# Optimization experiments

Measured on AMD Instinct MI355X. Metric: run time of the kernel, lower is better.

## Reference

```python
import jax, jax.numpy as jnp
import numpy as np

H = 128
B, N, K = 2, 16384, 16


def _gather_neighbors(a, idx):
    # a: (B,N,D), idx: (B,N,K) -> (B,N,K,D), per-batch gather along N
    return jax.vmap(lambda ab, ib: ab[ib])(a, idx)


def setup_inputs() -> dict:
    key = jax.random.key(0)
    ks = jax.random.split(key, 16)
    def lin(k, fan_in, shape):
        lim = 1.0 / np.sqrt(fan_in)
        return jax.random.uniform(k, shape, jnp.float32, -lim, lim)
    inp = {
        'h': jax.random.normal(ks[0], (B, N, H), jnp.float32),
        'x': jax.random.normal(ks[1], (B, N, 3), jnp.float32),
        'edge_idx': jax.random.randint(ks[2], (B, N, K), 0, N),
        # edge_mlp: Linear(2H+1->H), SiLU, Linear(H->H), SiLU
        'We1': lin(ks[3], 2 * H + 1, (2 * H + 1, H)), 'be1': lin(ks[4], 2 * H + 1, (H,)),
        'We2': lin(ks[5], H, (H, H)), 'be2': lin(ks[6], H, (H,)),
        # coord_mlp: Linear(H->H), SiLU, Linear(H->1, no bias)
        'Wc1': lin(ks[7], H, (H, H)), 'bc1': lin(ks[8], H, (H,)),
        'Wc2': lin(ks[9], H, (H, 1)),
        # node_mlp: Linear(2H->H), SiLU, Linear(H->H)
        'Wn1': lin(ks[10], 2 * H, (2 * H, H)), 'bn1': lin(ks[11], 2 * H, (H,)),
        'Wn2': lin(ks[12], H, (H, H)), 'bn2': lin(ks[13], H, (H,)),
    }
    return inp


def reference(h, x, edge_idx, We1, be1, We2, be2, Wc1, bc1, Wc2, Wn1, bn1, Wn2, bn2):
    k = edge_idx.shape[2]
    h_neigh = _gather_neighbors(h, edge_idx)          # (B,N,K,H)
    x_neigh = _gather_neighbors(x, edge_idx)          # (B,N,K,3)
    x_diff = x[:, :, None, :] - x_neigh               # (B,N,K,3)
    sq_dist = jnp.sum(x_diff * x_diff, axis=-1, keepdims=True)  # (B,N,K,1)
    h_i = jnp.broadcast_to(h[:, :, None, :], h_neigh.shape)
    edge_feat = jnp.concatenate([h_i, h_neigh, sq_dist], axis=-1)  # (B,N,K,2H+1)
    m_ij = jax.nn.silu(jax.nn.silu(edge_feat @ We1 + be1) @ We2 + be2)  # (B,N,K,H)
    coord_w = jax.nn.silu(m_ij @ Wc1 + bc1) @ Wc2     # (B,N,K,1)
    x_new = x + jnp.mean(x_diff * coord_w, axis=2)    # (B,N,3)
    m_i = jnp.sum(m_ij, axis=2)                       # (B,N,H)
    node_in = jnp.concatenate([h, m_i], axis=-1)      # (B,N,2H)
    h_new = jax.nn.silu(node_in @ Wn1 + bn1) @ Wn2 + bn2 + h
    return (h_new, x_new)
```

## Files before the change

### kernel.cpp

```cpp
#include <hip/hip_runtime.h>
#include <hip/hip_bf16.h>
#include <math.h>

#define H 128
#define KN 16
#define NN 16384
#define NB 8
#define EB 128
#define HS 136

typedef short s16x8 __attribute__((ext_vector_type(8)));
typedef float f32x4 __attribute__((ext_vector_type(4)));

__device__ __forceinline__ float u2f_lo(uint u){
    union { uint i; float f; } v; v.i = u << 16; return v.f;
}
__device__ __forceinline__ float u2f_hi(uint u){
    union { uint i; float f; } v; v.i = u & 0xffff0000u; return v.f;
}
__device__ __forceinline__ float b2f(ushort u){
    union { uint i; float f; } v; v.i = ((uint)u) << 16; return v.f;
}
__device__ __forceinline__ uint pk2(float lo, float hi){
    __hip_bfloat162 b = __float22bfloat162_rn(float2{lo, hi});
    uint u; __builtin_memcpy(&u, &b, 4); return u;
}
__device__ __forceinline__ ushort f2b1(float f){
    __hip_bfloat16 b = __float2bfloat16(f);
    ushort u; __builtin_memcpy(&u, &b, 2); return u;
}
__device__ __forceinline__ float silu_f(float v){
    float e = __expf(-v);
    return v * __builtin_amdgcn_rcpf(1.0f + e);
}

__global__ __launch_bounds__(256) void pack_all(
    const float* __restrict__ We2, const float* __restrict__ Wc1,
    const float* __restrict__ Wn1, const float* __restrict__ Wn2,
    const float* __restrict__ We1,
    ushort* __restrict__ dWe2, ushort* __restrict__ dWc1,
    ushort* __restrict__ dWn1, ushort* __restrict__ dWn2,
    ushort* __restrict__ dW1p)
{
    int idx = blockIdx.x * 256 + threadIdx.x;
    int fid = idx >> 6, l = idx & 63;
    const float* src; ushort* dst; int Kt; int mode = 0; int lfid;
    if (fid < 32)       { src = We2; dst = dWe2; Kt = 4; lfid = fid; }
    else if (fid < 64)  { src = Wc1; dst = dWc1; Kt = 4; lfid = fid - 32; }
    else if (fid < 128) { src = Wn1; dst = dWn1; Kt = 8; lfid = fid - 64; }
    else if (fid < 160) { src = Wn2; dst = dWn2; Kt = 4; lfid = fid - 128; }
    else                { src = We1; dst = dW1p; Kt = 4; mode = 1; lfid = fid - 160; }
    int mt = lfid / Kt, kt = lfid % Kt;
    int m = mt * 16 + (l & 15);
    s16x8 ov;
#pragma unroll
    for (int e = 0; e < 8; e++){
        int k = kt * 32 + ((l >> 4) << 3) + e;
        float v;
        if (mode == 0) v = src[k * 128 + m];
        else           v = src[(k + ((m >= 128) ? 128 : 0)) * 128 + (m & 127)];
        ov[e] = (short)f2b1(v);
    }
    *(s16x8*)(dst + (size_t)lfid * 512 + l * 8) = ov;
}

__global__ __launch_bounds__(256) void precompute_mfma(
    const float* __restrict__ h, const float* __restrict__ be1,
    const ushort* __restrict__ W1p,
    ushort* __restrict__ A, ushort* __restrict__ Bm)
{
    const int tid = threadIdx.x;
    const int w = tid >> 6, l = tid & 63, lg = l >> 4, li = l & 15;
    const int i0 = blockIdx.x * 64;

    f32x4 acc[4][4];
#pragma unroll
    for (int a = 0; a < 4; a++)
#pragma unroll
        for (int b = 0; b < 4; b++){ acc[a][b][0]=0.f; acc[a][b][1]=0.f; acc[a][b][2]=0.f; acc[a][b][3]=0.f; }

    for (int nt = 0; nt < 4; nt++){
        int node = i0 + nt * 16 + li;
        const float* hp = h + (size_t)node * 128 + lg * 8;
        s16x8 bfr[4];
#pragma unroll
        for (int kt = 0; kt < 4; kt++){
            float4 v0 = *(const float4*)(hp + kt * 32);
            float4 v1 = *(const float4*)(hp + kt * 32 + 4);
            uint4 uu = make_uint4(pk2(v0.x, v0.y), pk2(v0.z, v0.w),
                                  pk2(v1.x, v1.y), pk2(v1.z, v1.w));
            s16x8 bf; __builtin_memcpy(&bf, &uu, 16);
            bfr[kt] = bf;
        }
#pragma unroll
        for (int mtl = 0; mtl < 4; mtl++){
            int mt = w * 4 + mtl;
#pragma unroll
            for (int kt = 0; kt < 4; kt++){
                s16x8 af = *(const s16x8*)(W1p + (size_t)(mt * 4 + kt) * 512 + l * 8);
                acc[mtl][nt] = __builtin_amdgcn_mfma_f32_16x16x32_bf16(af, bfr[kt], acc[mtl][nt], 0, 0, 0);
            }
        }
    }
#pragma unroll
    for (int mtl = 0; mtl < 4; mtl++){
        int mt = w * 4 + mtl;
        int ccb = mt * 16 + lg * 4;
#pragma unroll
        for (int nt = 0; nt < 4; nt++){
            int node = i0 + nt * 16 + li;
            float b0=0.f,b1=0.f,b2=0.f,b3=0.f;
            if (ccb < 128){ float4 bb = *(const float4*)(be1 + ccb); b0=bb.x; b1=bb.y; b2=bb.z; b3=bb.w; }
            uint2 val = make_uint2(pk2(acc[mtl][nt][0] + b0, acc[mtl][nt][1] + b1),
                                   pk2(acc[mtl][nt][2] + b2, acc[mtl][nt][3] + b3));
            ushort* dst = (ccb < 128) ? (A + (size_t)node * 128 + ccb)
                                      : (Bm + (size_t)node * 128 + (ccb - 128));
            *(uint2*)dst = val;
        }
    }
}

__device__ __forceinline__ void gemm_pass(
    const ushort* mlds, const ushort* __restrict__ WT,
    int nt0, int w, int l, int lg, int li, f32x4 acc[2][4])
{
#pragma unroll
    for (int kt = 0; kt < 4; kt++){
        s16x8 bfr[4];
#pragma unroll
        for (int n = 0; n < 4; n++){
            int edge = (nt0 + n) * 16 + li;
            int blk = (kt * 4 + lg) ^ (edge & 7);
            bfr[n] = *(const s16x8*)&mlds[edge * 128 + blk * 8];
        }
#pragma unroll
        for (int mtl = 0; mtl < 2; mtl++){
            s16x8 af = *(const s16x8*)&WT[(size_t)((w * 2 + mtl) * 4 + kt) * 512 + l * 8];
#pragma unroll
            for (int n = 0; n < 4; n++)
                acc[mtl][n] = __builtin_amdgcn_mfma_f32_16x16x32_bf16(af, bfr[n], acc[mtl][n], 0, 0, 0);
        }
    }
}

__device__ __forceinline__ void m_epi(
    ushort* mlds, const float* __restrict__ be2,
    int nt0, int w, int lg, int li, f32x4 acc[2][4])
{
#pragma unroll
    for (int mtl = 0; mtl < 2; mtl++){
        int mt = w * 2 + mtl;
        int cb = mt * 16 + lg * 4;
        float4 bb = *(const float4*)&be2[cb];
#pragma unroll
        for (int n = 0; n < 4; n++){
            int el = (nt0 + n) * 16 + li;
            f32x4 a = acc[mtl][n];
            uint2 val = make_uint2(pk2(silu_f(a[0] + bb.x), silu_f(a[1] + bb.y)),
                                   pk2(silu_f(a[2] + bb.z), silu_f(a[3] + bb.w)));
            int blk = (mt * 2 + (lg >> 1)) ^ (el & 7);
            *(uint2*)&mlds[el * 128 + blk * 8 + (lg & 1) * 4] = val;
        }
    }
}

__device__ __forceinline__ void gemm2_pass(
    const ushort* mlds, const ushort* __restrict__ WT,
    const float* __restrict__ bc1, const float* __restrict__ Wc2,
    float* cwrow, int nt0, int w, int l, int lg, int li)
{
    f32x4 acc[2][4];
#pragma unroll
    for (int m = 0; m < 2; m++)
#pragma unroll
        for (int n = 0; n < 4; n++){ acc[m][n][0]=0.f; acc[m][n][1]=0.f; acc[m][n][2]=0.f; acc[m][n][3]=0.f; }

    __builtin_amdgcn_s_setprio(1);
    gemm_pass(mlds, WT, nt0, w, l, lg, li, acc);
    __builtin_amdgcn_s_setprio(0);

    float cwp[4] = {0.f, 0.f, 0.f, 0.f};
#pragma unroll
    for (int mtl = 0; mtl < 2; mtl++){
        int cb = (w * 2 + mtl) * 16 + lg * 4;
        float4 bc = *(const float4*)&bc1[cb];
        float4 wc = *(const float4*)&Wc2[cb];
#pragma unroll
        for (int n = 0; n < 4; n++){
            f32x4 a = acc[mtl][n];
            cwp[n] += silu_f(a[0] + bc.x) * wc.x + silu_f(a[1] + bc.y) * wc.y
                    + silu_f(a[2] + bc.z) * wc.z + silu_f(a[3] + bc.w) * wc.w;
        }
    }
#pragma unroll
    for (int n = 0; n < 4; n++){
        float v = cwp[n];
        v += __shfl_xor(v, 16);
        v += __shfl_xor(v, 32);
        if (lg == 0) cwrow[(nt0 + n) * 16 + li] = v;
    }
}

__global__ __launch_bounds__(256, 4) void egnn_fused(
    const float* __restrict__ h, const float* __restrict__ x,
    const int* __restrict__ edge_idx,
    const ushort* __restrict__ A, const ushort* __restrict__ Bm,
    const float* __restrict__ We1,
    const ushort* __restrict__ We2T, const float* __restrict__ be2,
    const ushort* __restrict__ Wc1T, const float* __restrict__ bc1,
    const float* __restrict__ Wc2,
    const ushort* __restrict__ Wn1T, const float* __restrict__ bn1,
    const ushort* __restrict__ Wn2T, const float* __restrict__ bn2,
    float* __restrict__ out, int BN)
{
    __shared__ __align__(16) ushort m_lds[EB * 128];
    __shared__ __align__(16) float  unionBuf[1056];
    __shared__ __align__(16) ushort hsh_bf[NB * HS];
    __shared__ float  sqd[EB];
    __shared__ ushort xdb[EB * 3];
    __shared__ ushort jgs[EB];

    float* Ashf = unionBuf;
    float (*cwvp)[EB] = (float(*)[EB])unionBuf;
    ushort* msum_bf = (ushort*)(unionBuf + 512);

    const int tid = threadIdx.x;
    const int w = tid >> 6, l = tid & 63, lg = l >> 4, li = l & 15;
    const int i0 = blockIdx.x * NB;

    {
        int r = tid >> 5, c = (tid & 31) * 4;
        float4 hv = *(const float4*)&h[(size_t)(i0 + r) * 128 + c];
        *(uint2*)&hsh_bf[r * HS + c] = make_uint2(pk2(hv.x, hv.y), pk2(hv.z, hv.w));
        uint2 av = *(const uint2*)&A[(size_t)(i0 + r) * 128 + c];
        float4 af;
        af.x = u2f_lo(av.x); af.y = u2f_hi(av.x);
        af.z = u2f_lo(av.y); af.w = u2f_hi(av.y);
        *(float4*)&Ashf[r * 128 + c] = af;
        if (tid < EB){
            int e = tid;
            int i = i0 + (e >> 4);
            int b = i / NN;
            int jl = edge_idx[(size_t)i * KN + (e & 15)];
            int j = b * NN + jl;
            jgs[e] = (ushort)j;
            float d0 = x[(size_t)i*3+0] - x[(size_t)j*3+0];
            float d1 = x[(size_t)i*3+1] - x[(size_t)j*3+1];
            float d2 = x[(size_t)i*3+2] - x[(size_t)j*3+2];
            xdb[e*3+0] = f2b1(d0); xdb[e*3+1] = f2b1(d1); xdb[e*3+2] = f2b1(d2);
            sqd[e] = d0*d0 + d1*d1 + d2*d2;
        }
    }
    __syncthreads();

    {
        const int e0 = w * 32;
        const float* w256 = We1 + 256 * 128;
#pragma unroll
        for (int nt = 0; nt < 2; nt++){
            int edge = e0 + nt * 16 + li;
            int nodel = edge >> 4;
            int j = jgs[edge];
            float sq = sqd[edge];
#pragma unroll
            for (int kt = 0; kt < 4; kt++){
                int c8 = kt * 32 + lg * 8;
                uint4 ub = *(const uint4*)&Bm[(size_t)j * 128 + c8];
                float4 a0 = *(const float4*)&Ashf[nodel * 128 + c8];
                float4 a1 = *(const float4*)&Ashf[nodel * 128 + c8 + 4];
                float4 w0 = *(const float4*)&w256[c8];
                float4 w1 = *(const float4*)&w256[c8 + 4];
                float alo[4] = {a0.x, a0.z, a1.x, a1.z};
                float ahi[4] = {a0.y, a0.w, a1.y, a1.w};
                float wlo[4] = {w0.x, w0.z, w1.x, w1.z};
                float whi[4] = {w0.y, w0.w, w1.y, w1.w};
                const uint* pb = (const uint*)&ub;
                uint ov[4];
#pragma unroll
                for (int p = 0; p < 4; p++){
                    float tlo = fmaf(sq, wlo[p], alo[p] + u2f_lo(pb[p]));
                    float thi = fmaf(sq, whi[p], ahi[p] + u2f_hi(pb[p]));
                    ov[p] = pk2(silu_f(tlo), silu_f(thi));
                }
                int blk = (kt * 4 + lg) ^ (edge & 7);
                *(uint4*)&m_lds[edge * 128 + blk * 8] = make_uint4(ov[0], ov[1], ov[2], ov[3]);
            }
        }
    }
    __syncthreads();

    {
        f32x4 acc[2][4];
#pragma unroll
        for (int m = 0; m < 2; m++)
#pragma unroll
            for (int n = 0; n < 4; n++){ acc[m][n][0]=0.f; acc[m][n][1]=0.f; acc[m][n][2]=0.f; acc[m][n][3]=0.f; }
        __builtin_amdgcn_s_setprio(1);
        gemm_pass(m_lds, We2T, 0, w, l, lg, li, acc);
        __builtin_amdgcn_s_setprio(0);
        __syncthreads();
        m_epi(m_lds, be2, 0, w, lg, li, acc);
    }
    {
        f32x4 acc[2][4];
#pragma unroll
        for (int m = 0; m < 2; m++)
#pragma unroll
            for (int n = 0; n < 4; n++){ acc[m][n][0]=0.f; acc[m][n][1]=0.f; acc[m][n][2]=0.f; acc[m][n][3]=0.f; }
        __builtin_amdgcn_s_setprio(1);
        gemm_pass(m_lds, We2T, 4, w, l, lg, li, acc);
        __builtin_amdgcn_s_setprio(0);
        __syncthreads();
        m_epi(m_lds, be2, 4, w, lg, li, acc);
    }

    {
        int nodel = l >> 3;
        int c0 = w * 32 + (l & 7) * 4;
        float s0=0.f, s1=0.f, s2=0.f, s3=0.f;
#pragma unroll
        for (int s = 0; s < 16; s++){
            int k = (s + nodel) & 15;
            int edge = nodel * 16 + k;
            int blk = (c0 >> 3) ^ (edge & 7);
            uint2 v = *(const uint2*)&m_lds[edge * 128 + blk * 8 + (c0 & 4)];
            s0 += u2f_lo(v.x); s1 += u2f_hi(v.x);
            s2 += u2f_lo(v.y); s3 += u2f_hi(v.y);
        }
        *(uint2*)&msum_bf[nodel * HS + c0] = make_uint2(pk2(s0, s1), pk2(s2, s3));
    }
    __syncthreads();

    gemm2_pass(m_lds, Wc1T, bc1, Wc2, cwvp[w], 0, w, l, lg, li);
    gemm2_pass(m_lds, Wc1T, bc1, Wc2, cwvp[w], 4, w, l, lg, li);
    __syncthreads();

    {
        f32x4 acc3[2];
        acc3[0][0]=0.f; acc3[0][1]=0.f; acc3[0][2]=0.f; acc3[0][3]=0.f;
        acc3[1][0]=0.f; acc3[1][1]=0.f; acc3[1][2]=0.f; acc3[1][3]=0.f;
        int node = li & 7;
#pragma unroll
        for (int kt = 0; kt < 8; kt++){
            const ushort* bp = (kt < 4) ? &hsh_bf[node * HS + kt * 32 + lg * 8]
                                        : &msum_bf[node * HS + (kt - 4) * 32 + lg * 8];
            s16x8 bf = *(const s16x8*)bp;
#pragma unroll
            for (int mtl = 0; mtl < 2; mtl++){
                int mt = w * 2 + mtl;
                s16x8 af = *(const s16x8*)&Wn1T[(size_t)(mt * 8 + kt) * 512 + l * 8];
                acc3[mtl] = __builtin_amdgcn_mfma_f32_16x16x32_bf16(af, bf, acc3[mtl], 0, 0, 0);
            }
        }
#pragma unroll
        for (int mtl = 0; mtl < 2; mtl++){
            int mt = w * 2 + mtl;
            int cb = mt * 16 + lg * 4;
            float4 bb = *(const float4*)&bn1[cb];
            uint o01 = 0, o23 = 0;
            if (li < 8){
                f32x4 a = acc3[mtl];
                o01 = pk2(silu_f(a[0] + bb.x), silu_f(a[1] + bb.y));
                o23 = pk2(silu_f(a[2] + bb.z), silu_f(a[3] + bb.w));
            }
            int blk = (mt * 2 + (lg >> 1)) ^ (li & 7);
            *(uint2*)&m_lds[li * 128 + blk * 8 + (lg & 1) * 4] = make_uint2(o01, o23);
        }
    }
    __syncthreads();

    if (tid < 24){
        int nd = tid / 3, d = tid % 3;
        int i = i0 + nd;
        float s = 0.f;
#pragma unroll
        for (int k = 0; k < 16; k++){
            int e = nd * 16 + k;
            float cw = cwvp[0][e] + cwvp[1][e] + cwvp[2][e] + cwvp[3][e];
            s += b2f(xdb[e * 3 + d]) * cw;
        }
        out[(size_t)BN * H + (size_t)i * 3 + d] = x[(size_t)i * 3 + d] + s * (1.0f / 16.0f);
    }

    {
        f32x4 acc4[2];
        acc4[0][0]=0.f; acc4[0][1]=0.f; acc4[0][2]=0.f; acc4[0][3]=0.f;
        acc4[1][0]=0.f; acc4[1][1]=0.f; acc4[1][2]=0.f; acc4[1][3]=0.f;
#pragma unroll
        for (int kt = 0; kt < 4; kt++){
            int blk = (kt * 4 + lg) ^ (li & 7);
            s16x8 bf = *(const s16x8*)&m_lds[li * 128 + blk * 8];
#pragma unroll
            for (int mtl = 0; mtl < 2; mtl++){
                int mt = w * 2 + mtl;
                s16x8 af = *(const s16x8*)&Wn2T[(size_t)(mt * 4 + kt) * 512 + l * 8];
                acc4[mtl] = __builtin_amdgcn_mfma_f32_16x16x32_bf16(af, bf, acc4[mtl], 0, 0, 0);
            }
        }
#pragma unroll
        for (int mtl = 0; mtl < 2; mtl++){
            int mt = w * 2 + mtl;
            int cb = mt * 16 + lg * 4;
            if (li < 8){
                float4 bb = *(const float4*)&bn2[cb];
                uint2 hu = *(const uint2*)&hsh_bf[li * HS + cb];
                f32x4 a = acc4[mtl];
                float4 o;
                o.x = a[0] + bb.x + u2f_lo(hu.x);
                o.y = a[1] + bb.y + u2f_hi(hu.x);
                o.z = a[2] + bb.z + u2f_lo(hu.y);
                o.w = a[3] + bb.w + u2f_hi(hu.y);
                *(float4*)&out[(size_t)(i0 + li) * 128 + cb] = o;
            }
        }
    }
}

extern "C" void kernel_launch(void* const* d_in, const int* in_sizes, int n_in,
                              void* d_out, int out_size, void* d_ws, size_t ws_size,
                              hipStream_t stream) {
    const float* h        = (const float*)d_in[0];
    const float* x        = (const float*)d_in[1];
    const int*   edge_idx = (const int*)d_in[2];
    const float* We1      = (const float*)d_in[3];
    const float* be1      = (const float*)d_in[4];
    const float* We2      = (const float*)d_in[5];
    const float* be2      = (const float*)d_in[6];
    const float* Wc1      = (const float*)d_in[7];
    const float* bc1      = (const float*)d_in[8];
    const float* Wc2      = (const float*)d_in[9];
    const float* Wn1      = (const float*)d_in[10];
    const float* bn1      = (const float*)d_in[11];
    const float* Wn2      = (const float*)d_in[12];
    const float* bn2      = (const float*)d_in[13];
    float* out = (float*)d_out;

    const int BN = in_sizes[0] / H;

    ushort* A    = (ushort*)d_ws;
    ushort* Bm   = A + (size_t)BN * H;
    ushort* We2T = Bm + (size_t)BN * H;
    ushort* Wc1T = We2T + 32 * 512;
    ushort* Wn1T = Wc1T + 32 * 512;
    ushort* Wn2T = Wn1T + 64 * 512;
    ushort* W1pT = Wn2T + 32 * 512;

    pack_all<<<56, 256, 0, stream>>>(We2, Wc1, Wn1, Wn2, We1,
                                     We2T, Wc1T, Wn1T, Wn2T, W1pT);
    precompute_mfma<<<BN / 64, 256, 0, stream>>>(h, be1, W1pT, A, Bm);
    egnn_fused<<<BN / NB, 256, 0, stream>>>(h, x, edge_idx, A, Bm, We1,
                                            We2T, be2, Wc1T, bc1, Wc2,
                                            Wn1T, bn1, Wn2T, bn2, out, BN);
}
```

Baseline: 120.4 us.

## Halve nodes per block to 4 and raise occupancy target to 5 blocks

Each block now handles 4 nodes (64 edges) instead of 8 (128), so every GEMM stage runs one pass instead of two and LDS use per block roughly halves. Launch bounds rise from 4 to 5 blocks per CU, and the edge-sum and coord stages are restructured around the smaller tile. The intent is more blocks in flight to hide gather latency. The cost is that node-level MFMAs use only 4 of 16 columns, wasting more compute, and twice as many blocks each reload the weights.

```diff
diff --git a/kernel.cpp b/kernel.cpp
--- a/kernel.cpp
+++ b/kernel.cpp
@@ -5,8 +5,8 @@
 #define H 128
 #define KN 16
 #define NN 16384
-#define NB 8
-#define EB 128
+#define NB 4
+#define EB 64
 #define HS 136
 
 typedef short s16x8 __attribute__((ext_vector_type(8)));
@@ -122,14 +122,14 @@
 
 __device__ __forceinline__ void gemm_pass(
     const ushort* mlds, const ushort* __restrict__ WT,
-    int nt0, int w, int l, int lg, int li, f32x4 acc[2][4])
+    int w, int l, int lg, int li, f32x4 acc[2][4])
 {
 #pragma unroll
     for (int kt = 0; kt < 4; kt++){
         s16x8 bfr[4];
 #pragma unroll
         for (int n = 0; n < 4; n++){
-            int edge = (nt0 + n) * 16 + li;
+            int edge = n * 16 + li;
             int blk = (kt * 4 + lg) ^ (edge & 7);
             bfr[n] = *(const s16x8*)&mlds[edge * 128 + blk * 8];
         }
@@ -145,7 +145,7 @@
 
 __device__ __forceinline__ void m_epi(
     ushort* mlds, const float* __restrict__ be2,
-    int nt0, int w, int lg, int li, f32x4 acc[2][4])
+    int w, int lg, int li, f32x4 acc[2][4])
 {
 #pragma unroll
     for (int mtl = 0; mtl < 2; mtl++){
@@ -154,7 +154,7 @@
         float4 bb = *(const float4*)&be2[cb];
 #pragma unroll
         for (int n = 0; n < 4; n++){
-            int el = (nt0 + n) * 16 + li;
+            int el = n * 16 + li;
             f32x4 a = acc[mtl][n];
             uint2 val = make_uint2(pk2(silu_f(a[0] + bb.x), silu_f(a[1] + bb.y)),
                                    pk2(silu_f(a[2] + bb.z), silu_f(a[3] + bb.w)));
@@ -164,44 +164,7 @@
     }
 }
 
-__device__ __forceinline__ void gemm2_pass(
-    const ushort* mlds, const ushort* __restrict__ WT,
-    const float* __restrict__ bc1, const float* __restrict__ Wc2,
-    float* cwrow, int nt0, int w, int l, int lg, int li)
-{
-    f32x4 acc[2][4];
-#pragma unroll
-    for (int m = 0; m < 2; m++)
-#pragma unroll
-        for (int n = 0; n < 4; n++){ acc[m][n][0]=0.f; acc[m][n][1]=0.f; acc[m][n][2]=0.f; acc[m][n][3]=0.f; }
-
-    __builtin_amdgcn_s_setprio(1);
-    gemm_pass(mlds, WT, nt0, w, l, lg, li, acc);
-    __builtin_amdgcn_s_setprio(0);
-
-    float cwp[4] = {0.f, 0.f, 0.f, 0.f};
-#pragma unroll
-    for (int mtl = 0; mtl < 2; mtl++){
-        int cb = (w * 2 + mtl) * 16 + lg * 4;
-        float4 bc = *(const float4*)&bc1[cb];
-        float4 wc = *(const float4*)&Wc2[cb];
-#pragma unroll
-        for (int n = 0; n < 4; n++){
-            f32x4 a = acc[mtl][n];
-            cwp[n] += silu_f(a[0] + bc.x) * wc.x + silu_f(a[1] + bc.y) * wc.y
-                    + silu_f(a[2] + bc.z) * wc.z + silu_f(a[3] + bc.w) * wc.w;
-        }
-    }
-#pragma unroll
-    for (int n = 0; n < 4; n++){
-        float v = cwp[n];
-        v += __shfl_xor(v, 16);
-        v += __shfl_xor(v, 32);
-        if (lg == 0) cwrow[(nt0 + n) * 16 + li] = v;
-    }
-}
-
-__global__ __launch_bounds__(256, 4) void egnn_fused(
+__global__ __launch_bounds__(256, 5) void egnn_fused(
     const float* __restrict__ h, const float* __restrict__ x,
     const int* __restrict__ edge_idx,
     const ushort* __restrict__ A, const ushort* __restrict__ Bm,
@@ -214,7 +177,7 @@
     float* __restrict__ out, int BN)
 {
     __shared__ __align__(16) ushort m_lds[EB * 128];
-    __shared__ __align__(16) float  unionBuf[1056];
+    __shared__ __align__(16) float  unionBuf[528];
     __shared__ __align__(16) ushort hsh_bf[NB * HS];
     __shared__ float  sqd[EB];
     __shared__ ushort xdb[EB * 3];
@@ -222,69 +185,67 @@
 
     float* Ashf = unionBuf;
     float (*cwvp)[EB] = (float(*)[EB])unionBuf;
-    ushort* msum_bf = (ushort*)(unionBuf + 512);
+    ushort* msum_bf = (ushort*)(unionBuf + 256);
 
     const int tid = threadIdx.x;
     const int w = tid >> 6, l = tid & 63, lg = l >> 4, li = l & 15;
     const int i0 = blockIdx.x * NB;
 
-    {
+    if (tid < 128){
         int r = tid >> 5, c = (tid & 31) * 4;
         float4 hv = *(const float4*)&h[(size_t)(i0 + r) * 128 + c];
         *(uint2*)&hsh_bf[r * HS + c] = make_uint2(pk2(hv.x, hv.y), pk2(hv.z, hv.w));
+    } else {
+        int t2 = tid - 128;
+        int r = t2 >> 5, c = (t2 & 31) * 4;
         uint2 av = *(const uint2*)&A[(size_t)(i0 + r) * 128 + c];
         float4 af;
         af.x = u2f_lo(av.x); af.y = u2f_hi(av.x);
         af.z = u2f_lo(av.y); af.w = u2f_hi(av.y);
         *(float4*)&Ashf[r * 128 + c] = af;
-        if (tid < EB){
-            int e = tid;
-            int i = i0 + (e >> 4);
-            int b = i / NN;
-            int jl = edge_idx[(size_t)i * KN + (e & 15)];
-            int j = b * NN + jl;
-            jgs[e] = (ushort)j;
-            float d0 = x[(size_t)i*3+0] - x[(size_t)j*3+0];
-            float d1 = x[(size_t)i*3+1] - x[(size_t)j*3+1];
-            float d2 = x[(size_t)i*3+2] - x[(size_t)j*3+2];
-            xdb[e*3+0] = f2b1(d0); xdb[e*3+1] = f2b1(d1); xdb[e*3+2] = f2b1(d2);
-            sqd[e] = d0*d0 + d1*d1 + d2*d2;
-        }
+    }
+    if (tid < EB){
+        int e = tid;
+        int i = i0 + (e >> 4);
+        int b = i / NN;
+        int jl = edge_idx[(size_t)i * KN + (e & 15)];
+        int j = b * NN + jl;
+        jgs[e] = (ushort)j;
+        float d0 = x[(size_t)i*3+0] - x[(size_t)j*3+0];
+        float d1 = x[(size_t)i*3+1] - x[(size_t)j*3+1];
+        float d2 = x[(size_t)i*3+2] - x[(size_t)j*3+2];
+        xdb[e*3+0] = f2b1(d0); xdb[e*3+1] = f2b1(d1); xdb[e*3+2] = f2b1(d2);
+        sqd[e] = d0*d0 + d1*d1 + d2*d2;
     }
     __syncthreads();
 
     {
-        const int e0 = w * 32;
         const float* w256 = We1 + 256 * 128;
-#pragma unroll
-        for (int nt = 0; nt < 2; nt++){
-            int edge = e0 + nt * 16 + li;
-            int nodel = edge >> 4;
-            int j = jgs[edge];
-            float sq = sqd[edge];
-#pragma unroll
-            for (int kt = 0; kt < 4; kt++){
-                int c8 = kt * 32 + lg * 8;
-                uint4 ub = *(const uint4*)&Bm[(size_t)j * 128 + c8];
-                float4 a0 = *(const float4*)&Ashf[nodel * 128 + c8];
-                float4 a1 = *(const float4*)&Ashf[nodel * 128 + c8 + 4];
-                float4 w0 = *(const float4*)&w256[c8];
-                float4 w1 = *(const float4*)&w256[c8 + 4];
-                float alo[4] = {a0.x, a0.z, a1.x, a1.z};
-                float ahi[4] = {a0.y, a0.w, a1.y, a1.w};
-                float wlo[4] = {w0.x, w0.z, w1.x, w1.z};
-                float whi[4] = {w0.y, w0.w, w1.y, w1.w};
-                const uint* pb = (const uint*)&ub;
-                uint ov[4];
-#pragma unroll
-                for (int p = 0; p < 4; p++){
-                    float tlo = fmaf(sq, wlo[p], alo[p] + u2f_lo(pb[p]));
-                    float thi = fmaf(sq, whi[p], ahi[p] + u2f_hi(pb[p]));
-                    ov[p] = pk2(silu_f(tlo), silu_f(thi));
-                }
-                int blk = (kt * 4 + lg) ^ (edge & 7);
-                *(uint4*)&m_lds[edge * 128 + blk * 8] = make_uint4(ov[0], ov[1], ov[2], ov[3]);
-            }
+        int edge = w * 16 + li;
+        int j = jgs[edge];
+        float sq = sqd[edge];
+#pragma unroll
+        for (int kt = 0; kt < 4; kt++){
+            int c8 = kt * 32 + lg * 8;
+            uint4 ub = *(const uint4*)&Bm[(size_t)j * 128 + c8];
+            float4 a0 = *(const float4*)&Ashf[w * 128 + c8];
+            float4 a1 = *(const float4*)&Ashf[w * 128 + c8 + 4];
+            float4 w0 = *(const float4*)&w256[c8];
+            float4 w1 = *(const float4*)&w256[c8 + 4];
+            float alo[4] = {a0.x, a0.z, a1.x, a1.z};
+            float ahi[4] = {a0.y, a0.w, a1.y, a1.w};
+            float wlo[4] = {w0.x, w0.z, w1.x, w1.z};
+            float whi[4] = {w0.y, w0.w, w1.y, w1.w};
+            const uint* pb = (const uint*)&ub;
+            uint ov[4];
+#pragma unroll
+            for (int p = 0; p < 4; p++){
+                float tlo = fmaf(sq, wlo[p], alo[p] + u2f_lo(pb[p]));
+                float thi = fmaf(sq, whi[p], ahi[p] + u2f_hi(pb[p]));
+                ov[p] = pk2(silu_f(tlo), silu_f(thi));
+            }
+            int blk = (kt * 4 + lg) ^ (edge & 7);
+            *(uint4*)&m_lds[edge * 128 + blk * 8] = make_uint4(ov[0], ov[1], ov[2], ov[3]);
         }
     }
     __syncthreads();
@@ -296,11 +257,27 @@
 #pragma unroll
             for (int n = 0; n < 4; n++){ acc[m][n][0]=0.f; acc[m][n][1]=0.f; acc[m][n][2]=0.f; acc[m][n][3]=0.f; }
         __builtin_amdgcn_s_setprio(1);
-        gemm_pass(m_lds, We2T, 0, w, l, lg, li, acc);
+        gemm_pass(m_lds, We2T, w, l, lg, li, acc);
         __builtin_amdgcn_s_setprio(0);
         __syncthreads();
-        m_epi(m_lds, be2, 0, w, lg, li, acc);
-    }
+        m_epi(m_lds, be2, w, lg, li, acc);
+    }
+
+    {
+        int node = l >> 4;
+        int c0 = w * 32 + (l & 15) * 2;
+        float s0 = 0.f, s1 = 0.f;
+#pragma unroll
+        for (int s = 0; s < 16; s++){
+            int k = (s + (l & 15)) & 15;
+            int edge = node * 16 + k;
+            uint v = *(const uint*)&m_lds[edge * 128 + ((c0 >> 3) ^ (edge & 7)) * 8 + (c0 & 6)];
+            s0 += u2f_lo(v); s1 += u2f_hi(v);
+        }
+        *(uint*)&msum_bf[node * HS + c0] = pk2(s0, s1);
+    }
+    __syncthreads();
+
     {
         f32x4 acc[2][4];
 #pragma unroll
@@ -308,38 +285,37 @@
 #pragma unroll
             for (int n = 0; n < 4; n++){ acc[m][n][0]=0.f; acc[m][n][1]=0.f; acc[m][n][2]=0.f; acc[m][n][3]=0.f; }
         __builtin_amdgcn_s_setprio(1);
-        gemm_pass(m_lds, We2T, 4, w, l, lg, li, acc);
+        gemm_pass(m_lds, Wc1T, w, l, lg, li, acc);
         __builtin_amdgcn_s_setprio(0);
-        __syncthreads();
-        m_epi(m_lds, be2, 4, w, lg, li, acc);
-    }
-
-    {
-        int nodel = l >> 3;
-        int c0 = w * 32 + (l & 7) * 4;
-        float s0=0.f, s1=0.f, s2=0.f, s3=0.f;
-#pragma unroll
-        for (int s = 0; s < 16; s++){
-            int k = (s + nodel) & 15;
-            int edge = nodel * 16 + k;
-            int blk = (c0 >> 3) ^ (edge & 7);
-            uint2 v = *(const uint2*)&m_lds[edge * 128 + blk * 8 + (c0 & 4)];
-            s0 += u2f_lo(v.x); s1 += u2f_hi(v.x);
-            s2 += u2f_lo(v.y); s3 += u2f_hi(v.y);
-        }
-        *(uint2*)&msum_bf[nodel * HS + c0] = make_uint2(pk2(s0, s1), pk2(s2, s3));
-    }
-    __syncthreads();
-
-    gemm2_pass(m_lds, Wc1T, bc1, Wc2, cwvp[w], 0, w, l, lg, li);
-    gemm2_pass(m_lds, Wc1T, bc1, Wc2, cwvp[w], 4, w, l, lg, li);
+
+        float cwp[4] = {0.f, 0.f, 0.f, 0.f};
+#pragma unroll
+        for (int mtl = 0; mtl < 2; mtl++){
+            int cb = (w * 2 + mtl) * 16 + lg * 4;
+            float4 bc = *(const float4*)&bc1[cb];
+            float4 wc = *(const float4*)&Wc2[cb];
+#pragma unroll
+            for (int n = 0; n < 4; n++){
+                f32x4 a = acc[mtl][n];
+                cwp[n] += silu_f(a[0] + bc.x) * wc.x + silu_f(a[1] + bc.y) * wc.y
+                        + silu_f(a[2] + bc.z) * wc.z + silu_f(a[3] + bc.w) * wc.w;
+            }
+        }
+#pragma unroll
+        for (int n = 0; n < 4; n++){
+            float v = cwp[n];
+            v += __shfl_xor(v, 16);
+            v += __shfl_xor(v, 32);
+            if (lg == 0) cwvp[w][n * 16 + li] = v;
+        }
+    }
     __syncthreads();
 
     {
         f32x4 acc3[2];
         acc3[0][0]=0.f; acc3[0][1]=0.f; acc3[0][2]=0.f; acc3[0][3]=0.f;
         acc3[1][0]=0.f; acc3[1][1]=0.f; acc3[1][2]=0.f; acc3[1][3]=0.f;
-        int node = li & 7;
+        int node = li & 3;
 #pragma unroll
         for (int kt = 0; kt < 8; kt++){
             const ushort* bp = (kt < 4) ? &hsh_bf[node * HS + kt * 32 + lg * 8]
@@ -358,7 +334,7 @@
             int cb = mt * 16 + lg * 4;
             float4 bb = *(const float4*)&bn1[cb];
             uint o01 = 0, o23 = 0;
-            if (li < 8){
+            if (li < 4){
                 f32x4 a = acc3[mtl];
                 o01 = pk2(silu_f(a[0] + bb.x), silu_f(a[1] + bb.y));
                 o23 = pk2(silu_f(a[2] + bb.z), silu_f(a[3] + bb.w));
@@ -369,7 +345,7 @@
     }
     __syncthreads();
 
-    if (tid < 24){
+    if (tid < 12){
         int nd = tid / 3, d = tid % 3;
         int i = i0 + nd;
         float s = 0.f;
@@ -401,7 +377,7 @@
         for (int mtl = 0; mtl < 2; mtl++){
             int mt = w * 2 + mtl;
             int cb = mt * 16 + lg * 4;
-            if (li < 8){
+            if (li < 4){
                 float4 bb = *(const float4*)&bn2[cb];
                 uint2 hu = *(const uint2*)&hsh_bf[li * HS + cb];
                 f32x4 a = acc4[mtl];
```

After: 134.6 us. 1.12x slower.

## Prefetch neighbor gathers into registers, drop staging barrier, swizzle blocks per XCD

Applied to the files above, without the earlier changes.

Each wave now loads its own edge indices, coordinate differences and gathered Bm rows straight into registers at kernel start, before the h/A staging loads. This removes the jgs/sqd shared arrays and the block-wide barrier that separated them from the first edge layer. The gather latency can then overlap with the staging work. Block IDs are also remapped so consecutive node groups land on the same XCD, which should improve L2 locality. The cost is extra VGPRs for the prefetched rows, which under the launch bounds of 256 threads and 4 blocks could cause spills or lower occupancy. Skipping the barrier relies on each wave reading only the Ashf rows it wrote itself.

```diff
diff --git a/kernel.cpp b/kernel.cpp
--- a/kernel.cpp
+++ b/kernel.cpp
@@ -216,9 +216,7 @@
     __shared__ __align__(16) ushort m_lds[EB * 128];
     __shared__ __align__(16) float  unionBuf[1056];
     __shared__ __align__(16) ushort hsh_bf[NB * HS];
-    __shared__ float  sqd[EB];
     __shared__ ushort xdb[EB * 3];
-    __shared__ ushort jgs[EB];
 
     float* Ashf = unionBuf;
     float (*cwvp)[EB] = (float(*)[EB])unionBuf;
@@ -226,7 +224,36 @@
 
     const int tid = threadIdx.x;
     const int w = tid >> 6, l = tid & 63, lg = l >> 4, li = l & 15;
-    const int i0 = blockIdx.x * NB;
+
+    int nwg = gridDim.x;
+    int per_xcd = nwg >> 3;
+    int phys = blockIdx.x;
+    int group = (phys & 7) * per_xcd + (phys >> 3);
+    const int i0 = group * NB;
+
+    int i_n0 = i0 + w * 2, i_n1 = i_n0 + 1;
+    int bb0 = i_n0 / NN;
+    int j0 = bb0 * NN + edge_idx[(size_t)i_n0 * KN + li];
+    int j1 = bb0 * NN + edge_idx[(size_t)i_n1 * KN + li];
+
+    float xi0x = x[(size_t)i_n0*3+0], xi0y = x[(size_t)i_n0*3+1], xi0z = x[(size_t)i_n0*3+2];
+    float xi1x = x[(size_t)i_n1*3+0], xi1y = x[(size_t)i_n1*3+1], xi1z = x[(size_t)i_n1*3+2];
+    float d00 = xi0x - x[(size_t)j0*3+0];
+    float d01 = xi0y - x[(size_t)j0*3+1];
+    float d02 = xi0z - x[(size_t)j0*3+2];
+    float d10 = xi1x - x[(size_t)j1*3+0];
+    float d11 = xi1y - x[(size_t)j1*3+1];
+    float d12 = xi1z - x[(size_t)j1*3+2];
+    float sq0 = d00*d00 + d01*d01 + d02*d02;
+    float sq1 = d10*d10 + d11*d11 + d12*d12;
+
+    uint4 bm0[4], bm1[4];
+#pragma unroll
+    for (int kt = 0; kt < 4; kt++){
+        int c8 = kt * 32 + lg * 8;
+        bm0[kt] = *(const uint4*)&Bm[(size_t)j0 * 128 + c8];
+        bm1[kt] = *(const uint4*)&Bm[(size_t)j1 * 128 + c8];
+    }
 
     {
         int r = tid >> 5, c = (tid & 31) * 4;
@@ -237,37 +264,26 @@
         af.x = u2f_lo(av.x); af.y = u2f_hi(av.x);
         af.z = u2f_lo(av.y); af.w = u2f_hi(av.y);
         *(float4*)&Ashf[r * 128 + c] = af;
-        if (tid < EB){
-            int e = tid;
-            int i = i0 + (e >> 4);
-            int b = i / NN;
-            int jl = edge_idx[(size_t)i * KN + (e & 15)];
-            int j = b * NN + jl;
-            jgs[e] = (ushort)j;
-            float d0 = x[(size_t)i*3+0] - x[(size_t)j*3+0];
-            float d1 = x[(size_t)i*3+1] - x[(size_t)j*3+1];
-            float d2 = x[(size_t)i*3+2] - x[(size_t)j*3+2];
-            xdb[e*3+0] = f2b1(d0); xdb[e*3+1] = f2b1(d1); xdb[e*3+2] = f2b1(d2);
-            sqd[e] = d0*d0 + d1*d1 + d2*d2;
-        }
-    }
-    __syncthreads();
-
-    {
-        const int e0 = w * 32;
+    }
+    if (lg == 0){
+        int e0 = w * 32 + li, e1 = e0 + 16;
+        xdb[e0*3+0] = f2b1(d00); xdb[e0*3+1] = f2b1(d01); xdb[e0*3+2] = f2b1(d02);
+        xdb[e1*3+0] = f2b1(d10); xdb[e1*3+1] = f2b1(d11); xdb[e1*3+2] = f2b1(d12);
+    }
+
+    {
         const float* w256 = We1 + 256 * 128;
 #pragma unroll
         for (int nt = 0; nt < 2; nt++){
-            int edge = e0 + nt * 16 + li;
-            int nodel = edge >> 4;
-            int j = jgs[edge];
-            float sq = sqd[edge];
+            int edge = w * 32 + nt * 16 + li;
+            float sq = nt ? sq1 : sq0;
+            int arow = (w * 2 + nt) * 128;
 #pragma unroll
             for (int kt = 0; kt < 4; kt++){
                 int c8 = kt * 32 + lg * 8;
-                uint4 ub = *(const uint4*)&Bm[(size_t)j * 128 + c8];
-                float4 a0 = *(const float4*)&Ashf[nodel * 128 + c8];
-                float4 a1 = *(const float4*)&Ashf[nodel * 128 + c8 + 4];
+                uint4 ub = nt ? bm1[kt] : bm0[kt];
+                float4 a0 = *(const float4*)&Ashf[arow + c8];
+                float4 a1 = *(const float4*)&Ashf[arow + c8 + 4];
                 float4 w0 = *(const float4*)&w256[c8];
                 float4 w1 = *(const float4*)&w256[c8 + 4];
                 float alo[4] = {a0.x, a0.z, a1.x, a1.z};
```

New measurement: 122.9 us. +2.1%, slower.

## Double fused-kernel tile to 16 nodes with 512 threads and XCD-aware block remap

Applied to the files above, without the earlier changes.

Each block now handles 16 nodes (256 edges) with 8 waves. Two half-blocks of 4 waves run the edge GEMMs on separate halves of the shared m buffer. The node-MLP MFMAs now fill all 16 columns instead of wasting half on padding, and the coordinate update runs on the idle waves in parallel with the final GEMM. Block indices are remapped so consecutive node groups land on the same XCD. LDS per block grows to roughly double, which may cut the number of resident blocks per CU.

```diff
diff --git a/kernel.cpp b/kernel.cpp
--- a/kernel.cpp
+++ b/kernel.cpp
@@ -5,8 +5,8 @@
 #define H 128
 #define KN 16
 #define NN 16384
-#define NB 8
-#define EB 128
+#define NB 16
+#define EB 256
 #define HS 136
 
 typedef short s16x8 __attribute__((ext_vector_type(8)));
@@ -121,21 +121,21 @@
 }
 
 __device__ __forceinline__ void gemm_pass(
-    const ushort* mlds, const ushort* __restrict__ WT,
-    int nt0, int w, int l, int lg, int li, f32x4 acc[2][4])
+    const ushort* mbase, const ushort* __restrict__ WT,
+    int nt0, int w4, int l, int lg, int li, f32x4 acc[2][4])
 {
 #pragma unroll
     for (int kt = 0; kt < 4; kt++){
         s16x8 bfr[4];
 #pragma unroll
         for (int n = 0; n < 4; n++){
-            int edge = (nt0 + n) * 16 + li;
-            int blk = (kt * 4 + lg) ^ (edge & 7);
-            bfr[n] = *(const s16x8*)&mlds[edge * 128 + blk * 8];
+            int el = (nt0 + n) * 16 + li;
+            int blk = (kt * 4 + lg) ^ (el & 7);
+            bfr[n] = *(const s16x8*)&mbase[el * 128 + blk * 8];
         }
 #pragma unroll
         for (int mtl = 0; mtl < 2; mtl++){
-            s16x8 af = *(const s16x8*)&WT[(size_t)((w * 2 + mtl) * 4 + kt) * 512 + l * 8];
+            s16x8 af = *(const s16x8*)&WT[(size_t)((w4 * 2 + mtl) * 4 + kt) * 512 + l * 8];
 #pragma unroll
             for (int n = 0; n < 4; n++)
                 acc[mtl][n] = __builtin_amdgcn_mfma_f32_16x16x32_bf16(af, bfr[n], acc[mtl][n], 0, 0, 0);
@@ -144,12 +144,12 @@
 }
 
 __device__ __forceinline__ void m_epi(
-    ushort* mlds, const float* __restrict__ be2,
-    int nt0, int w, int lg, int li, f32x4 acc[2][4])
+    ushort* mbase, const float* __restrict__ be2,
+    int nt0, int w4, int lg, int li, f32x4 acc[2][4])
 {
 #pragma unroll
     for (int mtl = 0; mtl < 2; mtl++){
-        int mt = w * 2 + mtl;
+        int mt = w4 * 2 + mtl;
         int cb = mt * 16 + lg * 4;
         float4 bb = *(const float4*)&be2[cb];
 #pragma unroll
@@ -159,15 +159,15 @@
             uint2 val = make_uint2(pk2(silu_f(a[0] + bb.x), silu_f(a[1] + bb.y)),
                                    pk2(silu_f(a[2] + bb.z), silu_f(a[3] + bb.w)));
             int blk = (mt * 2 + (lg >> 1)) ^ (el & 7);
-            *(uint2*)&mlds[el * 128 + blk * 8 + (lg & 1) * 4] = val;
+            *(uint2*)&mbase[el * 128 + blk * 8 + (lg & 1) * 4] = val;
         }
     }
 }
 
 __device__ __forceinline__ void gemm2_pass(
-    const ushort* mlds, const ushort* __restrict__ WT,
+    const ushort* mbase, const ushort* __restrict__ WT,
     const float* __restrict__ bc1, const float* __restrict__ Wc2,
-    float* cwrow, int nt0, int w, int l, int lg, int li)
+    int nt0, int w4, int l, int lg, int li, float cwp[4])
 {
     f32x4 acc[2][4];
 #pragma unroll
@@ -176,13 +176,13 @@
         for (int n = 0; n < 4; n++){ acc[m][n][0]=0.f; acc[m][n][1]=0.f; acc[m][n][2]=0.f; acc[m][n][3]=0.f; }
 
     __builtin_amdgcn_s_setprio(1);
-    gemm_pass(mlds, WT, nt0, w, l, lg, li, acc);
+    gemm_pass(mbase, WT, nt0, w4, l, lg, li, acc);
     __builtin_amdgcn_s_setprio(0);
 
-    float cwp[4] = {0.f, 0.f, 0.f, 0.f};
+    cwp[0]=0.f; cwp[1]=0.f; cwp[2]=0.f; cwp[3]=0.f;
 #pragma unroll
     for (int mtl = 0; mtl < 2; mtl++){
-        int cb = (w * 2 + mtl) * 16 + lg * 4;
+        int cb = (w4 * 2 + mtl) * 16 + lg * 4;
         float4 bc = *(const float4*)&bc1[cb];
         float4 wc = *(const float4*)&Wc2[cb];
 #pragma unroll
@@ -194,14 +194,12 @@
     }
 #pragma unroll
     for (int n = 0; n < 4; n++){
-        float v = cwp[n];
-        v += __shfl_xor(v, 16);
-        v += __shfl_xor(v, 32);
-        if (lg == 0) cwrow[(nt0 + n) * 16 + li] = v;
-    }
-}
-
-__global__ __launch_bounds__(256, 4) void egnn_fused(
+        cwp[n] += __shfl_xor(cwp[n], 16);
+        cwp[n] += __shfl_xor(cwp[n], 32);
+    }
+}
+
+__global__ __launch_bounds__(512, 4) void egnn_fused(
     const float* __restrict__ h, const float* __restrict__ x,
     const int* __restrict__ edge_idx,
     const ushort* __restrict__ A, const ushort* __restrict__ Bm,
@@ -214,19 +212,28 @@
     float* __restrict__ out, int BN)
 {
     __shared__ __align__(16) ushort m_lds[EB * 128];
-    __shared__ __align__(16) float  unionBuf[1056];
+    __shared__ __align__(16) float  unionBuf[2048];
     __shared__ __align__(16) ushort hsh_bf[NB * HS];
     __shared__ float  sqd[EB];
     __shared__ ushort xdb[EB * 3];
     __shared__ ushort jgs[EB];
 
     float* Ashf = unionBuf;
-    float (*cwvp)[EB] = (float(*)[EB])unionBuf;
-    ushort* msum_bf = (ushort*)(unionBuf + 512);
+    ushort* msum_bf = (ushort*)unionBuf;
+    float* cwv4 = (float*)(m_lds + 2048);
 
     const int tid = threadIdx.x;
     const int w = tid >> 6, l = tid & 63, lg = l >> 4, li = l & 15;
-    const int i0 = blockIdx.x * NB;
+    const int w4 = w & 3, half = w >> 2;
+    const int ebase = half * 128;
+
+    int nwg = gridDim.x;
+    int per_xcd = nwg >> 3;
+    int phys = blockIdx.x;
+    int group = (phys & 7) * per_xcd + (phys >> 3);
+    const int i0 = group * NB;
+
+    ushort* mhalf = m_lds + ebase * 128;
 
     {
         int r = tid >> 5, c = (tid & 31) * 4;
@@ -237,28 +244,27 @@
         af.x = u2f_lo(av.x); af.y = u2f_hi(av.x);
         af.z = u2f_lo(av.y); af.w = u2f_hi(av.y);
         *(float4*)&Ashf[r * 128 + c] = af;
-        if (tid < EB){
-            int e = tid;
-            int i = i0 + (e >> 4);
-            int b = i / NN;
-            int jl = edge_idx[(size_t)i * KN + (e & 15)];
-            int j = b * NN + jl;
-            jgs[e] = (ushort)j;
-            float d0 = x[(size_t)i*3+0] - x[(size_t)j*3+0];
-            float d1 = x[(size_t)i*3+1] - x[(size_t)j*3+1];
-            float d2 = x[(size_t)i*3+2] - x[(size_t)j*3+2];
-            xdb[e*3+0] = f2b1(d0); xdb[e*3+1] = f2b1(d1); xdb[e*3+2] = f2b1(d2);
-            sqd[e] = d0*d0 + d1*d1 + d2*d2;
-        }
+    }
+    if (tid < EB){
+        int e = tid;
+        int i = i0 + (e >> 4);
+        int b = i / NN;
+        int jl = edge_idx[(size_t)i * KN + (e & 15)];
+        int j = b * NN + jl;
+        jgs[e] = (ushort)j;
+        float d0 = x[(size_t)i*3+0] - x[(size_t)j*3+0];
+        float d1 = x[(size_t)i*3+1] - x[(size_t)j*3+1];
+        float d2 = x[(size_t)i*3+2] - x[(size_t)j*3+2];
+        xdb[e*3+0] = f2b1(d0); xdb[e*3+1] = f2b1(d1); xdb[e*3+2] = f2b1(d2);
+        sqd[e] = d0*d0 + d1*d1 + d2*d2;
     }
     __syncthreads();
 
     {
-        const int e0 = w * 32;
         const float* w256 = We1 + 256 * 128;
 #pragma unroll
         for (int nt = 0; nt < 2; nt++){
-            int edge = e0 + nt * 16 + li;
+            int edge = w * 32 + nt * 16 + li;
             int nodel = edge >> 4;
             int j = jgs[edge];
             float sq = sqd[edge];
@@ -296,10 +302,10 @@
 #pragma unroll
             for (int n = 0; n < 4; n++){ acc[m][n][0]=0.f; acc[m][n][1]=0.f; acc[m][n][2]=0.f; acc[m][n][3]=0.f; }
         __builtin_amdgcn_s_setprio(1);
-        gemm_pass(m_lds, We2T, 0, w, l, lg, li, acc);
+        gemm_pass(mhalf, We2T, 0, w4, l, lg, li, acc);
         __builtin_amdgcn_s_setprio(0);
         __syncthreads();
-        m_epi(m_lds, be2, 0, w, lg, li, acc);
+        m_epi(mhalf, be2, 0, w4, lg, li, acc);
     }
     {
         f32x4 acc[2][4];
@@ -308,42 +314,50 @@
 #pragma unroll
             for (int n = 0; n < 4; n++){ acc[m][n][0]=0.f; acc[m][n][1]=0.f; acc[m][n][2]=0.f; acc[m][n][3]=0.f; }
         __builtin_amdgcn_s_setprio(1);
-        gemm_pass(m_lds, We2T, 4, w, l, lg, li, acc);
+        gemm_pass(mhalf, We2T, 4, w4, l, lg, li, acc);
         __builtin_amdgcn_s_setprio(0);
         __syncthreads();
-        m_epi(m_lds, be2, 4, w, lg, li, acc);
+        m_epi(mhalf, be2, 4, w4, lg, li, acc);
     }
 
     {
-        int nodel = l >> 3;
-        int c0 = w * 32 + (l & 7) * 4;
+        int nd = half * 8 + (l >> 3);
+        int c0 = w4 * 32 + (l & 7) * 4;
         float s0=0.f, s1=0.f, s2=0.f, s3=0.f;
 #pragma unroll
         for (int s = 0; s < 16; s++){
-            int k = (s + nodel) & 15;
-            int edge = nodel * 16 + k;
+            int k = (s + (l >> 3)) & 15;
+            int edge = nd * 16 + k;
             int blk = (c0 >> 3) ^ (edge & 7);
             uint2 v = *(const uint2*)&m_lds[edge * 128 + blk * 8 + (c0 & 4)];
             s0 += u2f_lo(v.x); s1 += u2f_hi(v.x);
             s2 += u2f_lo(v.y); s3 += u2f_hi(v.y);
         }
-        *(uint2*)&msum_bf[nodel * HS + c0] = make_uint2(pk2(s0, s1), pk2(s2, s3));
+        *(uint2*)&msum_bf[nd * HS + c0] = make_uint2(pk2(s0, s1), pk2(s2, s3));
     }
     __syncthreads();
 
-    gemm2_pass(m_lds, Wc1T, bc1, Wc2, cwvp[w], 0, w, l, lg, li);
-    gemm2_pass(m_lds, Wc1T, bc1, Wc2, cwvp[w], 4, w, l, lg, li);
+    float cwpA[4], cwpB[4];
+    gemm2_pass(mhalf, Wc1T, bc1, Wc2, 0, w4, l, lg, li, cwpA);
+    gemm2_pass(mhalf, Wc1T, bc1, Wc2, 4, w4, l, lg, li, cwpB);
     __syncthreads();
 
-    {
+    if (lg == 0){
+#pragma unroll
+        for (int n = 0; n < 4; n++){
+            cwv4[w4 * EB + ebase + n * 16 + li]      = cwpA[n];
+            cwv4[w4 * EB + ebase + 64 + n * 16 + li] = cwpB[n];
+        }
+    }
+
+    if (w < 4){
         f32x4 acc3[2];
         acc3[0][0]=0.f; acc3[0][1]=0.f; acc3[0][2]=0.f; acc3[0][3]=0.f;
         acc3[1][0]=0.f; acc3[1][1]=0.f; acc3[1][2]=0.f; acc3[1][3]=0.f;
-        int node = li & 7;
 #pragma unroll
         for (int kt = 0; kt < 8; kt++){
-            const ushort* bp = (kt < 4) ? &hsh_bf[node * HS + kt * 32 + lg * 8]
-                                        : &msum_bf[node * HS + (kt - 4) * 32 + lg * 8];
+            const ushort* bp = (kt < 4) ? &hsh_bf[li * HS + kt * 32 + lg * 8]
+                                        : &msum_bf[li * HS + (kt - 4) * 32 + lg * 8];
             s16x8 bf = *(const s16x8*)bp;
 #pragma unroll
             for (int mtl = 0; mtl < 2; mtl++){
@@ -357,32 +371,16 @@
             int mt = w * 2 + mtl;
             int cb = mt * 16 + lg * 4;
             float4 bb = *(const float4*)&bn1[cb];
-            uint o01 = 0, o23 = 0;
-            if (li < 8){
-                f32x4 a = acc3[mtl];
-                o01 = pk2(silu_f(a[0] + bb.x), silu_f(a[1] + bb.y));
-                o23 = pk2(silu_f(a[2] + bb.z), silu_f(a[3] + bb.w));
-            }
+            f32x4 a = acc3[mtl];
+            uint o01 = pk2(silu_f(a[0] + bb.x), silu_f(a[1] + bb.y));
+            uint o23 = pk2(silu_f(a[2] + bb.z), silu_f(a[3] + bb.w));
             int blk = (mt * 2 + (lg >> 1)) ^ (li & 7);
             *(uint2*)&m_lds[li * 128 + blk * 8 + (lg & 1) * 4] = make_uint2(o01, o23);
         }
     }
     __syncthreads();
 
-    if (tid < 24){
-        int nd = tid / 3, d = tid % 3;
-        int i = i0 + nd;
-        float s = 0.f;
-#pragma unroll
-        for (int k = 0; k < 16; k++){
-            int e = nd * 16 + k;
-            float cw = cwvp[0][e] + cwvp[1][e] + cwvp[2][e] + cwvp[3][e];
-            s += b2f(xdb[e * 3 + d]) * cw;
-        }
-        out[(size_t)BN * H + (size_t)i * 3 + d] = x[(size_t)i * 3 + d] + s * (1.0f / 16.0f);
-    }
-
-    {
+    if (w < 4){
         f32x4 acc4[2];
         acc4[0][0]=0.f; acc4[0][1]=0.f; acc4[0][2]=0.f; acc4[0][3]=0.f;
         acc4[1][0]=0.f; acc4[1][1]=0.f; acc4[1][2]=0.f; acc4[1][3]=0.f;
@@ -401,17 +399,30 @@
         for (int mtl = 0; mtl < 2; mtl++){
             int mt = w * 2 + mtl;
             int cb = mt * 16 + lg * 4;
-            if (li < 8){
-                float4 bb = *(const float4*)&bn2[cb];
-                uint2 hu = *(const uint2*)&hsh_bf[li * HS + cb];
-                f32x4 a = acc4[mtl];
-                float4 o;
-                o.x = a[0] + bb.x + u2f_lo(hu.x);
-                o.y = a[1] + bb.y + u2f_hi(hu.x);
-                o.z = a[2] + bb.z + u2f_lo(hu.y);
-                o.w = a[3] + bb.w + u2f_hi(hu.y);
-                *(float4*)&out[(size_t)(i0 + li) * 128 + cb] = o;
+            float4 bb = *(const float4*)&bn2[cb];
+            uint2 hu = *(const uint2*)&hsh_bf[li * HS + cb];
+            f32x4 a = acc4[mtl];
+            float4 o;
+            o.x = a[0] + bb.x + u2f_lo(hu.x);
+            o.y = a[1] + bb.y + u2f_hi(hu.x);
+            o.z = a[2] + bb.z + u2f_lo(hu.y);
+            o.w = a[3] + bb.w + u2f_hi(hu.y);
+            *(float4*)&out[(size_t)(i0 + li) * 128 + cb] = o;
+        }
+    } else {
+        int idx = tid - 256;
+        if (idx < NB * 3){
+            int nd = idx / 3, d = idx % 3;
+            int i = i0 + nd;
+            float s = 0.f;
+#pragma unroll
+            for (int k = 0; k < 16; k++){
+                int e = nd * 16 + k;
+                float cw = cwv4[0 * EB + e] + cwv4[1 * EB + e]
+                         + cwv4[2 * EB + e] + cwv4[3 * EB + e];
+                s += b2f(xdb[e * 3 + d]) * cw;
             }
+            out[(size_t)BN * H + (size_t)i * 3 + d] = x[(size_t)i * 3 + d] + s * (1.0f / 16.0f);
         }
     }
 }
@@ -448,7 +459,7 @@
     pack_all<<<56, 256, 0, stream>>>(We2, Wc1, Wn1, Wn2, We1,
                                      We2T, Wc1T, Wn1T, Wn2T, W1pT);
     precompute_mfma<<<BN / 64, 256, 0, stream>>>(h, be1, W1pT, A, Bm);
-    egnn_fused<<<BN / NB, 256, 0, stream>>>(h, x, edge_idx, A, Bm, We1,
+    egnn_fused<<<BN / NB, 512, 0, stream>>>(h, x, edge_idx, A, Bm, We1,
                                             We2T, be2, Wc1T, bc1, Wc2,
                                             Wn1T, bn1, Wn2T, bn2, out, BN);
 }
```

New measurement: 123.2 us. 1.02x slower.
